# Kernel tuning notes

Measured on AMD Instinct MI355X. Metric: run time of the kernel, lower is better.

The kernel has to match this reference:

```python
import jax, jax.numpy as jnp
import numpy as np

D_MODEL = 1024
N_HEADS = 16
D_LATENT = 64
LN_EPS = 1e-5


def setup_inputs() -> dict:
    key = jax.random.key(0)
    ks = jax.random.split(key, 9)
    dm, h, dl = D_MODEL, N_HEADS, D_LATENT
    hd = h * dl
    # xavier_uniform with gain=0.1: limit = 0.1 * sqrt(6/(fan_in+fan_out))
    def xavier(k, fan_in, fan_out):
        lim = 0.1 * np.sqrt(6.0 / (fan_in + fan_out))
        return jax.random.uniform(k, (fan_in, fan_out), jnp.float32, -lim, lim)
    return {
        "x": jax.random.normal(ks[0], (4, 2048, dm), jnp.float32),
        "ln_g": jnp.ones((dm,), jnp.float32),
        "ln_b": jnp.zeros((dm,), jnp.float32),
        "wq": xavier(ks[1], dm, hd), "bq": jnp.zeros((hd,), jnp.float32),
        "wk": xavier(ks[2], dm, hd), "bk": jnp.zeros((hd,), jnp.float32),
        "wv": xavier(ks[3], dm, hd), "bv": jnp.zeros((hd,), jnp.float32),
        "wo": xavier(ks[4], hd, dm), "bo": jnp.zeros((dm,), jnp.float32),
    }


def reference(x, ln_g, ln_b, wq, bq, wk, bk, wv, bv, wo, bo):
    b, s, dm = x.shape
    h, dl = N_HEADS, D_LATENT
    # context = raw x (bound before LayerNorm in the torch code)
    context = x
    mu = jnp.mean(x, axis=-1, keepdims=True)
    var = jnp.var(x, axis=-1, keepdims=True)
    xn = (x - mu) * jax.lax.rsqrt(var + LN_EPS) * ln_g + ln_b
    q = (xn @ wq + bq).reshape(b, s, h, dl).transpose(0, 2, 1, 3)          # b h s d
    k = (context @ wk + bk).reshape(b, -1, h, dl).transpose(0, 2, 1, 3)    # b h t d
    v = (context @ wv + bv).reshape(b, -1, h, dl).transpose(0, 2, 1, 3)
    scores = jnp.einsum("bhsd,bhtd->bhst", q, k) / jnp.sqrt(jnp.float32(dl))
    attn = jax.nn.softmax(scores.astype(jnp.float32), axis=-1)
    # dropout omitted (eval mode / deterministic reference)
    out = jnp.einsum("bhst,bhtd->bhsd", attn, v)
    out = out.transpose(0, 2, 1, 3).reshape(b, s, h * dl)
    return out @ wo + bo
```

## Files before the change

### kernel.cpp

```cpp
#include <hip/hip_runtime.h>
#include <cstdint>

typedef __attribute__((ext_vector_type(8))) __bf16 bf16x8;
typedef __attribute__((ext_vector_type(8))) unsigned short u16x8;
typedef __attribute__((ext_vector_type(4))) unsigned short u16x4;
typedef __attribute__((ext_vector_type(4))) float f32x4;
typedef __attribute__((ext_vector_type(2))) unsigned int u32x2;
typedef __attribute__((ext_vector_type(4))) unsigned int u32x4;

__device__ inline unsigned short f2bf(float f) {
  return __builtin_bit_cast(unsigned short, (__bf16)f);
}

__device__ inline void llds16(const void* g, void* l) {
  __builtin_amdgcn_global_load_lds((const uint32_t*)g, (uint32_t*)l, 16, 0, 0);
}

__device__ inline bf16x8 ldfrag(const unsigned short* p) {
  u16x8 v = *(const u16x8*)p;
  return __builtin_bit_cast(bf16x8, v);
}

__device__ inline f32x4 mfma16(bf16x8 a, bf16x8 b, f32x4 c) {
  return __builtin_amdgcn_mfma_f32_16x16x32_bf16(a, b, c, 0, 0, 0);
}

__global__ __launch_bounds__(256) void prep_kernel(
    const float* __restrict__ x, const float* __restrict__ g, const float* __restrict__ be,
    unsigned short* __restrict__ xn, unsigned short* __restrict__ xb,
    const float* __restrict__ wq, const float* __restrict__ wk,
    const float* __restrict__ wv, const float* __restrict__ wo,
    unsigned short* __restrict__ wT, unsigned short* __restrict__ woT)
{
  __shared__ float t[64][66];
  const int tid = threadIdx.x;
  if (blockIdx.x < 8192) {
    const int row = blockIdx.x;
    const size_t base = (size_t)row * 1024 + tid * 4;
    float4 v = *(const float4*)&x[base];
    float s  = v.x + v.y + v.z + v.w;
    float sq = v.x*v.x + v.y*v.y + v.z*v.z + v.w*v.w;
#pragma unroll
    for (int o = 1; o < 64; o <<= 1) { s += __shfl_xor(s, o); sq += __shfl_xor(sq, o); }
    float* ls = &t[0][0];
    if ((tid & 63) == 0) { ls[tid >> 6] = s; ls[4 + (tid >> 6)] = sq; }
    __syncthreads();
    s  = ls[0] + ls[1] + ls[2] + ls[3];
    sq = ls[4] + ls[5] + ls[6] + ls[7];
    const float mu   = s * (1.f / 1024.f);
    const float var  = sq * (1.f / 1024.f) - mu * mu;
    const float rstd = rsqrtf(var + 1e-5f);
    float4 gv = *(const float4*)&g[tid * 4];
    float4 bv = *(const float4*)&be[tid * 4];
    u16x4 a, bb;
    a[0] = f2bf((v.x - mu) * rstd * gv.x + bv.x);
    a[1] = f2bf((v.y - mu) * rstd * gv.y + bv.y);
    a[2] = f2bf((v.z - mu) * rstd * gv.z + bv.z);
    a[3] = f2bf((v.w - mu) * rstd * gv.w + bv.w);
    bb[0] = f2bf(v.x); bb[1] = f2bf(v.y); bb[2] = f2bf(v.z); bb[3] = f2bf(v.w);
    *(u16x4*)&xn[base] = a;
    *(u16x4*)&xb[base] = bb;
  } else {
    const int zz = blockIdx.x - 8192;
    const int z = zz >> 8;
    const int rem = zz & 255;
    const int n0 = (rem & 15) * 64, k0 = (rem >> 4) * 64;
    const float* W = (z == 0) ? wq : (z == 1) ? wk : (z == 2) ? wv : wo;
    unsigned short* O = (z < 3) ? (wT + (size_t)z * 1048576) : woT;
    for (int idx = tid; idx < 1024; idx += 256) {
      int r = idx >> 4, c4 = (idx & 15) * 4;
      float4 w = *(const float4*)&W[(size_t)(k0 + r) * 1024 + n0 + c4];
      t[r][c4] = w.x; t[r][c4 + 1] = w.y; t[r][c4 + 2] = w.z; t[r][c4 + 3] = w.w;
    }
    __syncthreads();
    for (int idx = tid; idx < 1024; idx += 256) {
      int r = idx >> 4, c4 = (idx & 15) * 4;
      u16x4 pk;
#pragma unroll
      for (int j = 0; j < 4; j++) pk[j] = f2bf(t[c4 + j][r]);
      *(u16x4*)&O[(size_t)(n0 + r) * 1024 + k0 + c4] = pk;
    }
  }
}

template<int MODE>
__global__ __launch_bounds__(256) void gemm_kernel(
    const unsigned short* __restrict__ A0, const unsigned short* __restrict__ A1,
    const unsigned short* __restrict__ BT,
    const float* __restrict__ b0, const float* __restrict__ b1, const float* __restrict__ b2,
    void* __restrict__ Cv, int M, int N, int K)
{
  __shared__ unsigned short S[32768];
  const int tid = threadIdx.x;
  const int wave = tid >> 6, lane = tid & 63;
  const int l15 = lane & 15, l4 = lane >> 4;
  const int swz = (l15 & 7) << 3;
  const int NBN = N >> 7;
  const int nwg = gridDim.x, cpx = nwg >> 3;
  const int orig = blockIdx.x;
  const int id = (orig & 7) * cpx + (orig >> 3);
  const int grp = id / (NBN * 8);
  const int rem = id % (NBN * 8);
  const int bn = rem >> 3;
  const int bm = grp * 8 + (rem & 7);
  const int m0 = bm * 128, n0 = bn * 128;
  const unsigned short* Ap = (MODE == 0 && bn >= 8) ? A1 : A0;
  const int wr = (wave >> 1) * 64, wc = (wave & 1) * 64;

  f32x4 acc[4][4];
#pragma unroll
  for (int m = 0; m < 4; m++)
#pragma unroll
    for (int n = 0; n < 4; n++) acc[m][n] = {0.f, 0.f, 0.f, 0.f};

  auto STAGE = [&](int b, int kt) {
#pragma unroll
    for (int r = 0; r < 4; r++) {
      int D = r * 4096 + tid * 16;
      int row = D >> 7;
      int colus = ((D & 127) >> 1) ^ ((row & 7) << 3);
      llds16(&Ap[(size_t)(m0 + row) * K + kt + colus], &S[b * 16384 + r * 2048 + wave * 512]);
      llds16(&BT[(size_t)(n0 + row) * K + kt + colus],
             &S[b * 16384 + 8192 + r * 2048 + wave * 512]);
    }
  };

  const int KSTEPS = K >> 6;
  int cur = 0;
  STAGE(0, 0);
  for (int ki = 0; ki < KSTEPS; ki++) {
    if (ki < KSTEPS - 1) {
      STAGE(cur ^ 1, (ki + 1) << 6);
      asm volatile("s_waitcnt vmcnt(8)" ::: "memory");
    } else {
      asm volatile("s_waitcnt vmcnt(0)" ::: "memory");
    }
    __builtin_amdgcn_s_barrier();
    __builtin_amdgcn_sched_barrier(0);
    const unsigned short* Asb = &S[cur * 16384];
    const unsigned short* Bsb = &S[cur * 16384 + 8192];
#pragma unroll
    for (int ks = 0; ks < 2; ks++) {
      bf16x8 af[4], bfr[4];
#pragma unroll
      for (int m = 0; m < 4; m++)
        af[m]  = ldfrag(&Asb[(wr + m * 16 + l15) * 64 + ((ks * 32 + l4 * 8) ^ swz)]);
#pragma unroll
      for (int n = 0; n < 4; n++)
        bfr[n] = ldfrag(&Bsb[(wc + n * 16 + l15) * 64 + ((ks * 32 + l4 * 8) ^ swz)]);
#pragma unroll
      for (int m = 0; m < 4; m++)
#pragma unroll
        for (int n = 0; n < 4; n++)
          acc[m][n] = mfma16(af[m], bfr[n], acc[m][n]);
    }
    __builtin_amdgcn_s_barrier();
    cur ^= 1;
  }

#pragma unroll
  for (int nf = 0; nf < 4; nf++) {
    int c = n0 + wc + nf * 16 + l15;
    if (MODE == 0) {
      int sec = c >> 10;
      float bias = (sec == 0 ? b0 : (sec == 1 ? b1 : b2))[c & 1023];
      float sc = (sec == 0) ? 0.18033688011112042f : 1.0f;
      int h = (c >> 6) & 15, d = c & 63;
#pragma unroll
      for (int mf = 0; mf < 4; mf++) {
        int rbase = m0 + wr + mf * 16 + l4 * 4;
        int b = rbase >> 11, t = rbase & 2047;
        if (sec == 2) {
          u16x4 pk;
#pragma unroll
          for (int reg = 0; reg < 4; reg++) pk[reg] = f2bf(acc[mf][nf][reg] + bias);
          *(u16x4*)&((unsigned short*)Cv)[(size_t)2 * 8388608 +
                                          ((size_t)((b * 16 + h) * 64 + d)) * 2048 + t] = pk;
        } else {
#pragma unroll
          for (int reg = 0; reg < 4; reg++) {
            float v = acc[mf][nf][reg] + bias;
            ((unsigned short*)Cv)[(size_t)sec * 8388608 +
                                  ((size_t)(b * 16 + h) * 2048 + t + reg) * 64 + d] =
                f2bf(v * sc);
          }
        }
      }
    } else {
      float bias = b0[c];
#pragma unroll
      for (int mf = 0; mf < 4; mf++) {
#pragma unroll
        for (int reg = 0; reg < 4; reg++) {
          int rrow = m0 + wr + mf * 16 + l4 * 4 + reg;
          ((float*)Cv)[(size_t)rrow * N + c] = acc[mf][nf][reg] + bias;
        }
      }
    }
  }
}

__global__ __launch_bounds__(512, 4) void attn_kernel(
    const unsigned short* __restrict__ Q,
    const unsigned short* __restrict__ Kg,
    const unsigned short* __restrict__ VTg,
    unsigned short* __restrict__ Oa)
{
  __shared__ unsigned short S[32768];
  const int tid = threadIdx.x;
  const int wave = tid >> 6, lane = tid & 63;
  const int l15 = lane & 15, l4 = lane >> 4;
  const int swz = (l15 & 7) << 3;
  const int orig = blockIdx.x;
  const int wg = ((orig & 7) << 6) + (orig >> 3);
  const int qb = wg & 7, bh = wg >> 3;
  const size_t bhbase = (size_t)bh * 131072;
  const int q0 = qb * 256 + wave * 32;

  const u16x8 onesu = {0x3F80, 0x3F80, 0x3F80, 0x3F80, 0x3F80, 0x3F80, 0x3F80, 0x3F80};
  const bf16x8 ones = __builtin_bit_cast(bf16x8, onesu);

  bf16x8 qf[2][2];
#pragma unroll
  for (int m = 0; m < 2; m++)
#pragma unroll
    for (int ks = 0; ks < 2; ks++)
      qf[m][ks] = ldfrag(&Q[bhbase + (size_t)(q0 + m * 16 + l15) * 64 + ks * 32 + l4 * 8]);

  f32x4 accO[2][4];
#pragma unroll
  for (int m = 0; m < 2; m++)
#pragma unroll
    for (int n = 0; n < 4; n++) accO[m][n] = {0.f, 0.f, 0.f, 0.f};
  f32x4 accR[2] = {{0.f, 0.f, 0.f, 0.f}, {0.f, 0.f, 0.f, 0.f}};

  auto STAGE = [&](int b, int jj) {
#pragma unroll
    for (int r = 0; r < 2; r++) {
      int D = r * 8192 + tid * 16;
      int rowK = D >> 7;
      int colKus = ((D & 127) >> 1) ^ ((rowK & 7) << 3);
      llds16(&Kg[bhbase + (size_t)(jj * 128 + rowK) * 64 + colKus],
             &S[b * 16384 + r * 4096 + wave * 512]);
      int rowV = D >> 8;
      int colVus = ((D & 255) >> 1) ^ ((rowV & 7) << 3);
      llds16(&VTg[bhbase + (size_t)rowV * 2048 + jj * 128 + colVus],
             &S[b * 16384 + 8192 + r * 4096 + wave * 512]);
    }
  };

  int cur = 0;
  STAGE(0, 0);
  for (int j = 0; j < 16; j++) {
    if (j < 15) {
      STAGE(cur ^ 1, j + 1);
      asm volatile("s_waitcnt vmcnt(4)" ::: "memory");
    } else {
      asm volatile("s_waitcnt vmcnt(0)" ::: "memory");
    }
    __builtin_amdgcn_s_barrier();
    __builtin_amdgcn_sched_barrier(0);

    const unsigned short* Kb = &S[cur * 16384];
    const unsigned short* Vb = &S[cur * 16384 + 8192];

#pragma unroll
    for (int kt = 0; kt < 4; kt++) {
      bf16x8 kf00 = ldfrag(&Kb[((2 * kt) * 16 + l15) * 64 + ((0 * 32 + l4 * 8) ^ swz)]);
      bf16x8 kf01 = ldfrag(&Kb[((2 * kt) * 16 + l15) * 64 + ((1 * 32 + l4 * 8) ^ swz)]);
      bf16x8 kf10 = ldfrag(&Kb[((2 * kt + 1) * 16 + l15) * 64 + ((0 * 32 + l4 * 8) ^ swz)]);
      bf16x8 kf11 = ldfrag(&Kb[((2 * kt + 1) * 16 + l15) * 64 + ((1 * 32 + l4 * 8) ^ swz)]);
      f32x4 sa = {0.f, 0.f, 0.f, 0.f}, sb = sa, sc = sa, sd = sa;
      __builtin_amdgcn_s_setprio(1);
      sa = mfma16(kf00, qf[0][0], sa); sb = mfma16(kf00, qf[1][0], sb);
      sc = mfma16(kf10, qf[0][0], sc); sd = mfma16(kf10, qf[1][0], sd);
      sa = mfma16(kf01, qf[0][1], sa); sb = mfma16(kf01, qf[1][1], sb);
      sc = mfma16(kf11, qf[0][1], sc); sd = mfma16(kf11, qf[1][1], sd);
      __builtin_amdgcn_s_setprio(0);

      bf16x8 vf[4];
#pragma unroll
      for (int n = 0; n < 4; n++)
        vf[n] = ldfrag(&Vb[(n * 16 + l15) * 128 + ((kt * 32 + l4 * 8) ^ swz)]);

      bf16x8 pf[2];
#pragma unroll
      for (int m = 0; m < 2; m++) {
        const f32x4 se = (m == 0) ? sa : sb;
        const f32x4 so = (m == 0) ? sc : sd;
        uint32_t V0, V1, V2, V3;
        {
          u16x4 pk;
#pragma unroll
          for (int r = 0; r < 4; r++) pk[r] = f2bf(__builtin_amdgcn_exp2f(se[r]));
          u32x2 w = __builtin_bit_cast(u32x2, pk);
          V0 = w[0]; V1 = w[1];
        }
        {
          u16x4 pk;
#pragma unroll
          for (int r = 0; r < 4; r++) pk[r] = f2bf(__builtin_amdgcn_exp2f(so[r]));
          u32x2 w = __builtin_bit_cast(u32x2, pk);
          V2 = w[0]; V3 = w[1];
        }
        asm("s_nop 1\n\t"
            "v_permlane32_swap_b32 %0, %2\n\t"
            "v_permlane32_swap_b32 %1, %3\n\t"
            "v_permlane16_swap_b32 %0, %2\n\t"
            "v_permlane16_swap_b32 %1, %3"
            : "+v"(V0), "+v"(V1), "+v"(V2), "+v"(V3));
        u32x4 fw = {V0, V1, V2, V3};
        pf[m] = __builtin_bit_cast(bf16x8, fw);
      }

      __builtin_amdgcn_s_setprio(1);
#pragma unroll
      for (int m = 0; m < 2; m++) {
        accR[m] = mfma16(pf[m], ones, accR[m]);
#pragma unroll
        for (int n = 0; n < 4; n++)
          accO[m][n] = mfma16(pf[m], vf[n], accO[m][n]);
      }
      __builtin_amdgcn_s_setprio(0);
    }

    __builtin_amdgcn_s_barrier();
    cur ^= 1;
  }

  const int b = bh >> 4, h = bh & 15;
#pragma unroll
  for (int m = 0; m < 2; m++)
#pragma unroll
    for (int reg = 0; reg < 4; reg++) {
      float inv = 1.0f / accR[m][reg];
      int srow = q0 + m * 16 + l4 * 4 + reg;
#pragma unroll
      for (int n = 0; n < 4; n++) {
        float v = accO[m][n][reg] * inv;
        Oa[((size_t)(b * 2048) + srow) * 1024 + h * 64 + n * 16 + l15] = f2bf(v);
      }
    }
}

extern "C" void kernel_launch(void* const* d_in, const int* in_sizes, int n_in,
                              void* d_out, int out_size, void* d_ws, size_t ws_size,
                              hipStream_t stream) {
  (void)in_sizes; (void)n_in; (void)out_size; (void)ws_size;
  const float* x   = (const float*)d_in[0];
  const float* lng = (const float*)d_in[1];
  const float* lnb = (const float*)d_in[2];
  const float* wq  = (const float*)d_in[3];
  const float* bq  = (const float*)d_in[4];
  const float* wk  = (const float*)d_in[5];
  const float* bk  = (const float*)d_in[6];
  const float* wv  = (const float*)d_in[7];
  const float* bv  = (const float*)d_in[8];
  const float* wo  = (const float*)d_in[9];
  const float* bo  = (const float*)d_in[10];

  unsigned short* ws = (unsigned short*)d_ws;
  const size_t NE = 8388608;
  unsigned short* xn  = ws;
  unsigned short* xb  = ws + NE;
  unsigned short* wT  = ws + 2 * NE;
  unsigned short* woT = wT + 3145728;
  unsigned short* qkv = woT + 1048576;
  unsigned short* oat = xb;

  prep_kernel<<<dim3(9216), 256, 0, stream>>>(x, lng, lnb, xn, xb, wq, wk, wv, wo, wT, woT);
  gemm_kernel<0><<<dim3(1536), 256, 0, stream>>>(xn, xb, wT, bq, bk, bv, qkv, 8192, 3072, 1024);
  attn_kernel<<<dim3(512), 512, 0, stream>>>(qkv, qkv + NE, qkv + 2 * NE, oat);
  gemm_kernel<1><<<dim3(512), 256, 0, stream>>>(oat, oat, woT, bo, bo, bo, d_out, 8192, 1024, 1024);
}
```

Measured before the change: 170.4 us.

## Replace double-buffered LDS pipeline with single buffer and raise MFMA priority

```diff
diff --git a/kernel.cpp b/kernel.cpp
--- a/kernel.cpp
+++ b/kernel.cpp
@@ -90,7 +90,7 @@
     const float* __restrict__ b0, const float* __restrict__ b1, const float* __restrict__ b2,
     void* __restrict__ Cv, int M, int N, int K)
 {
-  __shared__ unsigned short S[32768];
+  __shared__ unsigned short S[16384];
   const int tid = threadIdx.x;
   const int wave = tid >> 6, lane = tid & 63;
   const int l15 = lane & 15, l4 = lane >> 4;
@@ -113,49 +113,39 @@
 #pragma unroll
     for (int n = 0; n < 4; n++) acc[m][n] = {0.f, 0.f, 0.f, 0.f};
 
-  auto STAGE = [&](int b, int kt) {
+  auto STAGE = [&](int kt) {
 #pragma unroll
     for (int r = 0; r < 4; r++) {
       int D = r * 4096 + tid * 16;
       int row = D >> 7;
       int colus = ((D & 127) >> 1) ^ ((row & 7) << 3);
-      llds16(&Ap[(size_t)(m0 + row) * K + kt + colus], &S[b * 16384 + r * 2048 + wave * 512]);
-      llds16(&BT[(size_t)(n0 + row) * K + kt + colus],
-             &S[b * 16384 + 8192 + r * 2048 + wave * 512]);
+      llds16(&Ap[(size_t)(m0 + row) * K + kt + colus], &S[r * 2048 + wave * 512]);
+      llds16(&BT[(size_t)(n0 + row) * K + kt + colus], &S[8192 + r * 2048 + wave * 512]);
     }
   };
 
   const int KSTEPS = K >> 6;
-  int cur = 0;
-  STAGE(0, 0);
   for (int ki = 0; ki < KSTEPS; ki++) {
-    if (ki < KSTEPS - 1) {
-      STAGE(cur ^ 1, (ki + 1) << 6);
-      asm volatile("s_waitcnt vmcnt(8)" ::: "memory");
-    } else {
-      asm volatile("s_waitcnt vmcnt(0)" ::: "memory");
-    }
-    __builtin_amdgcn_s_barrier();
-    __builtin_amdgcn_sched_barrier(0);
-    const unsigned short* Asb = &S[cur * 16384];
-    const unsigned short* Bsb = &S[cur * 16384 + 8192];
+    __syncthreads();
+    STAGE(ki << 6);
+    __syncthreads();
 #pragma unroll
     for (int ks = 0; ks < 2; ks++) {
       bf16x8 af[4], bfr[4];
 #pragma unroll
       for (int m = 0; m < 4; m++)
-        af[m]  = ldfrag(&Asb[(wr + m * 16 + l15) * 64 + ((ks * 32 + l4 * 8) ^ swz)]);
+        af[m]  = ldfrag(&S[(wr + m * 16 + l15) * 64 + ((ks * 32 + l4 * 8) ^ swz)]);
 #pragma unroll
       for (int n = 0; n < 4; n++)
-        bfr[n] = ldfrag(&Bsb[(wc + n * 16 + l15) * 64 + ((ks * 32 + l4 * 8) ^ swz)]);
+        bfr[n] = ldfrag(&S[8192 + (wc + n * 16 + l15) * 64 + ((ks * 32 + l4 * 8) ^ swz)]);
+      __builtin_amdgcn_s_setprio(1);
 #pragma unroll
       for (int m = 0; m < 4; m++)
 #pragma unroll
         for (int n = 0; n < 4; n++)
           acc[m][n] = mfma16(af[m], bfr[n], acc[m][n]);
-    }
-    __builtin_amdgcn_s_barrier();
-    cur ^= 1;
+      __builtin_amdgcn_s_setprio(0);
+    }
   }
 
 #pragma unroll
```

Measured after the change: 179.6 us. 5.4% more time.
